# Performance work log

Measured on AMD Instinct MI355X. Metric: run time of the kernel, lower is better.

Reference implementation:

```python
import jax, jax.numpy as jnp
import numpy as np

# Model constants (from init_kwargs)
D, P, M_STEPS, H = 32, 8, 50, 128
INTERVAL, SIGMA = 1.0, 1.0
N = 32768


def setup_inputs() -> dict:
    key = jax.random.key(0)
    ks = jax.random.split(key, 7)
    return {
        "observations": jax.random.normal(ks[0], (P,), jnp.float32),
        "initial_states": jax.random.normal(ks[1], (N, D), jnp.float32),
        "initial_values": jax.random.normal(ks[2], (N,), jnp.float32),
        "noise": jax.random.normal(ks[3], (M_STEPS, N, D), jnp.float32),
        "W1": jax.random.normal(ks[4], (D + P + 2, H), jnp.float32) * 0.05,
        "b1": jnp.zeros((H,), jnp.float32),
        "W2": jax.random.normal(ks[5], (H, D), jnp.float32) * 0.05,
        "b2": jnp.zeros((D,), jnp.float32),
        "theta": jax.random.uniform(ks[6], (1,), jnp.float32, 0.1, 1.0),
        "obs_index": 3,
        "control_required": 1,
    }


def reference(observations, initial_states, initial_values, noise,
              W1, b1, W2, b2, theta, obs_index, control_required):
    dt = jnp.float32(INTERVAL / M_STEPS)
    sqrt_dt = jnp.sqrt(dt)
    times = jnp.linspace(0.0, INTERVAL, M_STEPS + 1, dtype=jnp.float32)[:M_STEPS]
    n = initial_states.shape[0]
    Yb = jnp.broadcast_to(observations, (n, P))          # (N, p)
    t_feat = jnp.full((n, 1), float(obs_index), jnp.float32)
    cr = jnp.float32(control_required)

    def z_net(s, X):
        # Z_Network: MLP over [X, Y, s, t] -> (N, d)
        feats = jnp.concatenate([X, Yb, jnp.full((n, 1), s, jnp.float32), t_feat], axis=1)
        h = jnp.tanh(feats @ W1 + b1)
        return h @ W2 + b2

    def step(carry, xs):
        X, V = carry
        noise_m, s = xs
        W = sqrt_dt * noise_m                            # Brownian increment (N, d)
        Z = z_net(s, X)                                  # (N, d)
        control = -jax.lax.stop_gradient(Z) * cr         # detach + flag
        drift_V = 0.5 * jnp.sum(jnp.square(Z), axis=1) + jnp.sum(control * Z, axis=1)
        V = V + dt * drift_V + jnp.sum(Z * W, axis=1)
        drift_X = -theta * X + SIGMA * control           # b(theta, X) = -theta * X (OU drift)
        X = X + dt * drift_X + SIGMA * W
        return (X, V), None

    (X, V), _ = jax.lax.scan(step, (initial_states, initial_values), (noise, times))
    return X, V
```

## Files before the change

kernel.cpp:

```cpp
#include <hip/hip_runtime.h>
#include <math.h>

#define NPART 32768
#define MS 50
#define BLOCK 256

typedef __attribute__((ext_vector_type(8))) short bfrag;
typedef __attribute__((ext_vector_type(4))) float ffrag;

__device__ __forceinline__ unsigned short f2bf(float x) {
    unsigned u = __float_as_uint(x);
    u += 0x7fffu + ((u >> 16) & 1u);
    return (unsigned short)(u >> 16);
}

__device__ __forceinline__ unsigned pk2(float a, float b) {
    unsigned r;
    asm("v_cvt_pk_bf16_f32 %0, %1, %2" : "=v"(r) : "v"(a), "v"(b));
    return r;
}

__device__ __forceinline__ float nexp2(float x) {
#if __has_builtin(__builtin_amdgcn_exp2f)
    return __builtin_amdgcn_exp2f(x);
#else
    float r;
    asm("v_exp_f32 %0, %1" : "=v"(r) : "v"(x));
    return r;
#endif
}
__device__ __forceinline__ float nrcp(float x) {
#if __has_builtin(__builtin_amdgcn_rcpf)
    return __builtin_amdgcn_rcpf(x);
#else
    float r;
    asm("v_rcp_f32 %0, %1" : "=v"(r) : "v"(x));
    return r;
#endif
}

__device__ __forceinline__ float fast_tanh(float x) {
    const float c = 2.8853900817779268f;
    float e = nexp2(x * c);
    float r = nrcp(e + 1.0f);
    return fmaf(-2.0f, r, 1.0f);
}

__global__ __launch_bounds__(BLOCK, 2)
void fused_sde_mfma(const float* __restrict__ obs,
                    const float* __restrict__ x0,
                    const float* __restrict__ v0,
                    const float* __restrict__ noise,
                    const float* __restrict__ gW1,
                    const float* __restrict__ gb1,
                    const float* __restrict__ gW2,
                    const float* __restrict__ gb2,
                    const float* __restrict__ gtheta,
                    const int* __restrict__ gobs_idx,
                    const int* __restrict__ gctrl,
                    float* __restrict__ outX,
                    float* __restrict__ outV)
{
    __shared__ __align__(16) float Zlds[4][16][36];

    const int tid  = threadIdx.x;
    const int w    = tid >> 6;
    const int lane = tid & 63;
    const int p    = lane & 15;
    const int q    = lane >> 4;
    const int part = blockIdx.x * 64 + w * 16 + p;

    const float theta = gtheta[0];
    const float tfeat = (float)gobs_idx[0];
    const float cr    = (float)gctrl[0];
    const float dt      = 1.0f / (float)MS;
    const float sqrt_dt = sqrtf(dt);
    const float ax  = 1.0f - dt * theta;
    const float bcr = dt * cr;
    const float kv  = dt * (0.5f - cr);

    bfrag A1[8];
    #pragma unroll
    for (int mt = 0; mt < 8; ++mt) {
        const int h = 16 * mt + p;
        bfrag a;
        #pragma unroll
        for (int j = 0; j < 8; ++j)
            a[j] = (short)f2bf(gW1[(8 * q + j) * 128 + h]);
        A1[mt] = a;
    }

    bfrag B2[2][4];
    #pragma unroll
    for (int nt = 0; nt < 2; ++nt) {
        #pragma unroll
        for (int kt = 0; kt < 4; ++kt) {
            bfrag b;
            #pragma unroll
            for (int j = 0; j < 8; ++j) {
                const int h = 32 * kt + 16 * (j >> 2) + 4 * q + (j & 3);
                b[j] = (short)f2bf(gW2[h * 32 + 16 * nt + p]);
            }
            B2[nt][kt] = b;
        }
    }

    ffrag Stat[8], W1s[8];
    #pragma unroll
    for (int mt = 0; mt < 8; ++mt) {
        #pragma unroll
        for (int r = 0; r < 4; ++r) {
            const int h = 16 * mt + 4 * q + r;
            float acc = gb1[h];
            #pragma unroll
            for (int j = 0; j < 8; ++j)
                acc = fmaf(obs[j], gW1[(32 + j) * 128 + h], acc);
            acc = fmaf(tfeat, gW1[41 * 128 + h], acc);
            Stat[mt][r] = acc;
            W1s[mt][r]  = gW1[40 * 128 + h];
        }
    }

    const float bz0 = gb2[p], bz1 = gb2[16 + p];
    const ffrag Z0i = ffrag{bz0, bz0, bz0, bz0};
    const ffrag Z1i = ffrag{bz1, bz1, bz1, bz1};
    const ffrag Zzero = ffrag{0.f, 0.f, 0.f, 0.f};

    float X[8];
    {
        const float4* xp = (const float4*)(x0 + (size_t)part * 32 + 8 * q);
        float4 a = xp[0], b = xp[1];
        X[0] = a.x; X[1] = a.y; X[2] = a.z; X[3] = a.w;
        X[4] = b.x; X[5] = b.y; X[6] = b.z; X[7] = b.w;
    }
    float V = v0[part];

    const float* nbase = noise + (size_t)part * 32 + 8 * q;
    float4 nc0 = ((const float4*)nbase)[0];
    float4 nc1 = ((const float4*)nbase)[1];

    float* zbase = &Zlds[w][0][0];
    const float* zrow = &Zlds[w][p][0];

    #pragma unroll 1
    for (int m = 0; m < MS; ++m) {
        const int mn = (m + 1 < MS) ? m + 1 : m;
        const float* np = nbase + (size_t)mn * ((size_t)NPART * 32);
        float4 nn0 = ((const float4*)np)[0];
        float4 nn1 = ((const float4*)np)[1];

        int4 bxw = make_int4((int)pk2(X[0], X[1]), (int)pk2(X[2], X[3]),
                             (int)pk2(X[4], X[5]), (int)pk2(X[6], X[7]));
        bfrag BX = __builtin_bit_cast(bfrag, bxw);

        const float s = (float)m * dt;

        ffrag C[8];
        #pragma unroll
        for (int mt = 0; mt < 8; ++mt) {
            ffrag c;
            #pragma unroll
            for (int r = 0; r < 4; ++r) c[r] = fmaf(s, W1s[mt][r], Stat[mt][r]);
            C[mt] = c;
        }
        #pragma unroll
        for (int mt = 0; mt < 8; ++mt)
            C[mt] = __builtin_amdgcn_mfma_f32_16x16x32_bf16(A1[mt], BX, C[mt], 0, 0, 0);

        uint2 Hpk[8];
        #pragma unroll
        for (int mt = 0; mt < 8; ++mt) {
            const unsigned u0 = pk2(fast_tanh(C[mt][0]), fast_tanh(C[mt][1]));
            const unsigned u1 = pk2(fast_tanh(C[mt][2]), fast_tanh(C[mt][3]));
            Hpk[mt] = make_uint2(u0, u1);
        }

        ffrag D0a = Z0i, D0b = Zzero, D1a = Z1i, D1b = Zzero;
        #pragma unroll
        for (int kt = 0; kt < 4; ++kt) {
            int4 aw = make_int4((int)Hpk[2 * kt].x, (int)Hpk[2 * kt].y,
                                (int)Hpk[2 * kt + 1].x, (int)Hpk[2 * kt + 1].y);
            bfrag A = __builtin_bit_cast(bfrag, aw);
            if (kt & 1) {
                D0b = __builtin_amdgcn_mfma_f32_16x16x32_bf16(A, B2[0][kt], D0b, 0, 0, 0);
                D1b = __builtin_amdgcn_mfma_f32_16x16x32_bf16(A, B2[1][kt], D1b, 0, 0, 0);
            } else {
                D0a = __builtin_amdgcn_mfma_f32_16x16x32_bf16(A, B2[0][kt], D0a, 0, 0, 0);
                D1a = __builtin_amdgcn_mfma_f32_16x16x32_bf16(A, B2[1][kt], D1a, 0, 0, 0);
            }
        }
        ffrag D0 = D0a + D0b;
        ffrag D1 = D1a + D1b;

        #pragma unroll
        for (int r = 0; r < 4; ++r) {
            float* zr = zbase + (4 * q + r) * 36;
            zr[p]      = D0[r];
            zr[16 + p] = D1[r];
        }

        __builtin_amdgcn_wave_barrier();

        float4 z0 = *(const float4*)&zrow[8 * q];
        float4 z1 = *(const float4*)&zrow[8 * q + 4];
        float Z[8] = {z0.x, z0.y, z0.z, z0.w, z1.x, z1.y, z1.z, z1.w};
        float Nn[8] = {nc0.x, nc0.y, nc0.z, nc0.w, nc1.x, nc1.y, nc1.z, nc1.w};

        float s2 = 0.0f, sn = 0.0f;
        #pragma unroll
        for (int j = 0; j < 8; ++j) {
            s2 = fmaf(Z[j], Z[j], s2);
            sn = fmaf(Z[j], Nn[j], sn);
        }
        s2 += __shfl_xor(s2, 16); s2 += __shfl_xor(s2, 32);
        sn += __shfl_xor(sn, 16); sn += __shfl_xor(sn, 32);
        V = fmaf(kv, s2, fmaf(sqrt_dt, sn, V));

        #pragma unroll
        for (int j = 0; j < 8; ++j) {
            float t = fmaf(-bcr, Z[j], sqrt_dt * Nn[j]);
            X[j] = fmaf(ax, X[j], t);
        }

        nc0 = nn0; nc1 = nn1;

        __builtin_amdgcn_wave_barrier();
    }

    float4* xout = (float4*)(outX + (size_t)part * 32 + 8 * q);
    xout[0] = make_float4(X[0], X[1], X[2], X[3]);
    xout[1] = make_float4(X[4], X[5], X[6], X[7]);
    if (q == 0) outV[part] = V;
}

extern "C" void kernel_launch(void* const* d_in, const int* in_sizes, int n_in,
                              void* d_out, int out_size, void* d_ws, size_t ws_size,
                              hipStream_t stream) {
    const float* obs   = (const float*)d_in[0];
    const float* x0    = (const float*)d_in[1];
    const float* v0    = (const float*)d_in[2];
    const float* noise = (const float*)d_in[3];
    const float* W1    = (const float*)d_in[4];
    const float* b1    = (const float*)d_in[5];
    const float* W2    = (const float*)d_in[6];
    const float* b2    = (const float*)d_in[7];
    const float* th    = (const float*)d_in[8];
    const int*   oi    = (const int*)d_in[9];
    const int*   cr    = (const int*)d_in[10];

    float* outX = (float*)d_out;
    float* outV = outX + (size_t)NPART * 32;

    dim3 grid(NPART / 64);
    fused_sde_mfma<<<grid, BLOCK, 0, stream>>>(obs, x0, v0, noise, W1, b1, W2, b2,
                                               th, oi, cr, outX, outV);
}
```

Before: 313.2 us.

## Split hidden dimension across wave pairs with LDS reduction of Z

```diff
diff --git a/kernel.cpp b/kernel.cpp
--- a/kernel.cpp
+++ b/kernel.cpp
@@ -46,7 +46,7 @@
     return fmaf(-2.0f, r, 1.0f);
 }
 
-__global__ __launch_bounds__(BLOCK, 2)
+__global__ __launch_bounds__(BLOCK, 4)
 void fused_sde_mfma(const float* __restrict__ obs,
                     const float* __restrict__ x0,
                     const float* __restrict__ v0,
@@ -65,10 +65,12 @@
 
     const int tid  = threadIdx.x;
     const int w    = tid >> 6;
+    const int g    = w & 1;
+    const int hh   = w >> 1;
     const int lane = tid & 63;
     const int p    = lane & 15;
     const int q    = lane >> 4;
-    const int part = blockIdx.x * 64 + w * 16 + p;
+    const int part = blockIdx.x * 32 + g * 16 + p;
 
     const float theta = gtheta[0];
     const float tfeat = (float)gobs_idx[0];
@@ -79,10 +81,10 @@
     const float bcr = dt * cr;
     const float kv  = dt * (0.5f - cr);
 
-    bfrag A1[8];
+    bfrag A1[4];
     #pragma unroll
-    for (int mt = 0; mt < 8; ++mt) {
-        const int h = 16 * mt + p;
+    for (int mt = 0; mt < 4; ++mt) {
+        const int h = 64 * hh + 16 * mt + p;
         bfrag a;
         #pragma unroll
         for (int j = 0; j < 8; ++j)
@@ -90,27 +92,28 @@
         A1[mt] = a;
     }
 
-    bfrag B2[2][4];
+    bfrag B2[2][2];
     #pragma unroll
     for (int nt = 0; nt < 2; ++nt) {
         #pragma unroll
-        for (int kt = 0; kt < 4; ++kt) {
+        for (int ktl = 0; ktl < 2; ++ktl) {
+            const int kt = 2 * hh + ktl;
             bfrag b;
             #pragma unroll
             for (int j = 0; j < 8; ++j) {
                 const int h = 32 * kt + 16 * (j >> 2) + 4 * q + (j & 3);
                 b[j] = (short)f2bf(gW2[h * 32 + 16 * nt + p]);
             }
-            B2[nt][kt] = b;
-        }
-    }
-
-    ffrag Stat[8], W1s[8];
+            B2[nt][ktl] = b;
+        }
+    }
+
+    ffrag Stat[4], W1s[4];
     #pragma unroll
-    for (int mt = 0; mt < 8; ++mt) {
+    for (int mt = 0; mt < 4; ++mt) {
         #pragma unroll
         for (int r = 0; r < 4; ++r) {
-            const int h = 16 * mt + 4 * q + r;
+            const int h = 64 * hh + 16 * mt + 4 * q + r;
             float acc = gb1[h];
             #pragma unroll
             for (int j = 0; j < 8; ++j)
@@ -121,10 +124,10 @@
         }
     }
 
-    const float bz0 = gb2[p], bz1 = gb2[16 + p];
+    const float bz0 = (hh == 0) ? gb2[p]      : 0.0f;
+    const float bz1 = (hh == 0) ? gb2[16 + p] : 0.0f;
     const ffrag Z0i = ffrag{bz0, bz0, bz0, bz0};
     const ffrag Z1i = ffrag{bz1, bz1, bz1, bz1};
-    const ffrag Zzero = ffrag{0.f, 0.f, 0.f, 0.f};
 
     float X[8];
     {
@@ -133,14 +136,15 @@
         X[0] = a.x; X[1] = a.y; X[2] = a.z; X[3] = a.w;
         X[4] = b.x; X[5] = b.y; X[6] = b.z; X[7] = b.w;
     }
-    float V = v0[part];
+    float V = (hh == 0) ? v0[part] : 0.0f;
 
     const float* nbase = noise + (size_t)part * 32 + 8 * q;
     float4 nc0 = ((const float4*)nbase)[0];
     float4 nc1 = ((const float4*)nbase)[1];
 
     float* zbase = &Zlds[w][0][0];
-    const float* zrow = &Zlds[w][p][0];
+    const float* zrow0 = &Zlds[g][p][0];
+    const float* zrow1 = &Zlds[2 + g][p][0];
 
     #pragma unroll 1
     for (int m = 0; m < MS; ++m) {
@@ -155,42 +159,35 @@
 
         const float s = (float)m * dt;
 
-        ffrag C[8];
-        #pragma unroll
-        for (int mt = 0; mt < 8; ++mt) {
+        ffrag C[4];
+        #pragma unroll
+        for (int mt = 0; mt < 4; ++mt) {
             ffrag c;
             #pragma unroll
             for (int r = 0; r < 4; ++r) c[r] = fmaf(s, W1s[mt][r], Stat[mt][r]);
             C[mt] = c;
         }
         #pragma unroll
-        for (int mt = 0; mt < 8; ++mt)
+        for (int mt = 0; mt < 4; ++mt)
             C[mt] = __builtin_amdgcn_mfma_f32_16x16x32_bf16(A1[mt], BX, C[mt], 0, 0, 0);
 
-        uint2 Hpk[8];
-        #pragma unroll
-        for (int mt = 0; mt < 8; ++mt) {
+        uint2 Hpk[4];
+        #pragma unroll
+        for (int mt = 0; mt < 4; ++mt) {
             const unsigned u0 = pk2(fast_tanh(C[mt][0]), fast_tanh(C[mt][1]));
             const unsigned u1 = pk2(fast_tanh(C[mt][2]), fast_tanh(C[mt][3]));
             Hpk[mt] = make_uint2(u0, u1);
         }
 
-        ffrag D0a = Z0i, D0b = Zzero, D1a = Z1i, D1b = Zzero;
-        #pragma unroll
-        for (int kt = 0; kt < 4; ++kt) {
-            int4 aw = make_int4((int)Hpk[2 * kt].x, (int)Hpk[2 * kt].y,
-                                (int)Hpk[2 * kt + 1].x, (int)Hpk[2 * kt + 1].y);
+        ffrag D0 = Z0i, D1 = Z1i;
+        #pragma unroll
+        for (int ktl = 0; ktl < 2; ++ktl) {
+            int4 aw = make_int4((int)Hpk[2 * ktl].x, (int)Hpk[2 * ktl].y,
+                                (int)Hpk[2 * ktl + 1].x, (int)Hpk[2 * ktl + 1].y);
             bfrag A = __builtin_bit_cast(bfrag, aw);
-            if (kt & 1) {
-                D0b = __builtin_amdgcn_mfma_f32_16x16x32_bf16(A, B2[0][kt], D0b, 0, 0, 0);
-                D1b = __builtin_amdgcn_mfma_f32_16x16x32_bf16(A, B2[1][kt], D1b, 0, 0, 0);
-            } else {
-                D0a = __builtin_amdgcn_mfma_f32_16x16x32_bf16(A, B2[0][kt], D0a, 0, 0, 0);
-                D1a = __builtin_amdgcn_mfma_f32_16x16x32_bf16(A, B2[1][kt], D1a, 0, 0, 0);
-            }
-        }
-        ffrag D0 = D0a + D0b;
-        ffrag D1 = D1a + D1b;
+            D0 = __builtin_amdgcn_mfma_f32_16x16x32_bf16(A, B2[0][ktl], D0, 0, 0, 0);
+            D1 = __builtin_amdgcn_mfma_f32_16x16x32_bf16(A, B2[1][ktl], D1, 0, 0, 0);
+        }
 
         #pragma unroll
         for (int r = 0; r < 4; ++r) {
@@ -199,22 +196,27 @@
             zr[16 + p] = D1[r];
         }
 
-        __builtin_amdgcn_wave_barrier();
-
-        float4 z0 = *(const float4*)&zrow[8 * q];
-        float4 z1 = *(const float4*)&zrow[8 * q + 4];
-        float Z[8] = {z0.x, z0.y, z0.z, z0.w, z1.x, z1.y, z1.z, z1.w};
+        __syncthreads();
+
+        float4 a0 = *(const float4*)&zrow0[8 * q];
+        float4 a1 = *(const float4*)&zrow0[8 * q + 4];
+        float4 b0 = *(const float4*)&zrow1[8 * q];
+        float4 b1 = *(const float4*)&zrow1[8 * q + 4];
+        float Z[8] = {a0.x + b0.x, a0.y + b0.y, a0.z + b0.z, a0.w + b0.w,
+                      a1.x + b1.x, a1.y + b1.y, a1.z + b1.z, a1.w + b1.w};
         float Nn[8] = {nc0.x, nc0.y, nc0.z, nc0.w, nc1.x, nc1.y, nc1.z, nc1.w};
 
-        float s2 = 0.0f, sn = 0.0f;
-        #pragma unroll
-        for (int j = 0; j < 8; ++j) {
-            s2 = fmaf(Z[j], Z[j], s2);
-            sn = fmaf(Z[j], Nn[j], sn);
-        }
-        s2 += __shfl_xor(s2, 16); s2 += __shfl_xor(s2, 32);
-        sn += __shfl_xor(sn, 16); sn += __shfl_xor(sn, 32);
-        V = fmaf(kv, s2, fmaf(sqrt_dt, sn, V));
+        if (hh == 0) {
+            float s2 = 0.0f, sn = 0.0f;
+            #pragma unroll
+            for (int j = 0; j < 8; ++j) {
+                s2 = fmaf(Z[j], Z[j], s2);
+                sn = fmaf(Z[j], Nn[j], sn);
+            }
+            s2 += __shfl_xor(s2, 16); s2 += __shfl_xor(s2, 32);
+            sn += __shfl_xor(sn, 16); sn += __shfl_xor(sn, 32);
+            V = fmaf(kv, s2, fmaf(sqrt_dt, sn, V));
+        }
 
         #pragma unroll
         for (int j = 0; j < 8; ++j) {
@@ -224,13 +226,15 @@
 
         nc0 = nn0; nc1 = nn1;
 
-        __builtin_amdgcn_wave_barrier();
-    }
-
-    float4* xout = (float4*)(outX + (size_t)part * 32 + 8 * q);
-    xout[0] = make_float4(X[0], X[1], X[2], X[3]);
-    xout[1] = make_float4(X[4], X[5], X[6], X[7]);
-    if (q == 0) outV[part] = V;
+        __syncthreads();
+    }
+
+    if (hh == 0) {
+        float4* xout = (float4*)(outX + (size_t)part * 32 + 8 * q);
+        xout[0] = make_float4(X[0], X[1], X[2], X[3]);
+        xout[1] = make_float4(X[4], X[5], X[6], X[7]);
+        if (q == 0) outV[part] = V;
+    }
 }
 
 extern "C" void kernel_launch(void* const* d_in, const int* in_sizes, int n_in,
@@ -251,7 +255,7 @@
     float* outX = (float*)d_out;
     float* outV = outX + (size_t)NPART * 32;
 
-    dim3 grid(NPART / 64);
+    dim3 grid(NPART / 32);
     fused_sde_mfma<<<grid, BLOCK, 0, stream>>>(obs, x0, v0, noise, W1, b1, W2, b2,
                                                th, oi, cr, outX, outV);
 }
```

After: 396.7 us. 26.6% more time.
